# Kernel tuning notes

Hardware: AMD Instinct MI355X
Metric: run time of the kernel (lower is better)

## Reference

```python
import jax, jax.numpy as jnp
import numpy as np

# ---- module constants (from init_kwargs) ----
NOF_LINKS = 64
NOISE = 1e-3          # gen_para.input_noise_power
DT = 0.01             # gen_para.dt
T_END = 5.12          # t
TXP = 1.0             # gen_para.tx_power
LAM = 1.0
RHO = 1.0

T_ARR = jnp.arange(0.0, T_END, DT, dtype=jnp.float32)   # [T] time grid
POW2T = jnp.power(jnp.float32(2.0), T_ARR)               # 2^t
POW2T_1 = POW2T - 1.0                                    # 2^t - 1
LN2 = jnp.log(jnp.float32(2.0))


def setup_inputs() -> dict:
    key = jax.random.key(0)
    k1, k2 = jax.random.split(key)
    pathloss = jax.random.uniform(k1, (NOF_LINKS, NOF_LINKS), dtype=jnp.float32)
    powers = jax.random.uniform(k2, (16, 20, NOF_LINKS), dtype=jnp.float32)
    return {"pathloss": pathloss, "powers": powers}


def _outage(pathloss, power):
    # power: [B, N, L]; pathloss: [L, L]
    B, N, L = power.shape
    T = T_ARR.shape[0]
    # signal[b,n,i,j] = pathloss[i,j] * power[b,n,i]  (per original expand/permute)
    y_ii = jnp.diagonal(pathloss)[None, None, :] * power              # [B,N,L]
    y_tot = power * jnp.sum(pathloss, axis=1)[None, None, :]          # sum_j signal
    y_ij = y_tot - y_ii
    sinr = y_ii / (y_ij + NOISE)                                      # [B,N,L]

    # block-0 outage CDF over time grid: Q1[b,i,t] = 1 - exp(-(2^t-1) * sinr[b,0,i])
    Q1 = 1.0 - jnp.exp(-POW2T_1[None, None, :] * sinr[:, 0, :, None])  # [B,L,T]

    # per-block pdf kernels for n >= 1 (vectorized over all blocks up front)
    s = sinr[:, 1:, :, None]                                          # [B,N-1,L,1]
    q = jnp.exp(-POW2T_1 * s) * POW2T * s * LN2                       # [B,N-1,L,T]

    def step(Q, qn):
        # Q, qn: [B,L,T]; per-channel grouped cross-correlation (torch conv1d semantics)
        x = Q.reshape(1, B * L, T)
        w = qn.reshape(B * L, 1, T)
        out = jax.lax.conv_general_dilated(
            x, w, window_strides=(1,), padding=[(T - 1, T - 1)],
            feature_group_count=B * L)                                 # [1,B*L,2T-1]
        Qn = out[0, :, :T].reshape(B, L, T) * DT
        return Qn, Qn[:, :, -1]

    q_scan = jnp.moveaxis(q, 1, 0)                                    # [N-1,B,L,T]
    _, outa_rest = jax.lax.scan(step, Q1, q_scan)                     # [N-1,B,L]
    outa = jnp.concatenate([Q1[None, :, :, -1], outa_rest], axis=0)   # [N,B,L]
    return jnp.moveaxis(outa, 0, 1)                                   # [B,N,L]


def reference(pathloss, powers):
    power = powers * TXP
    N = power.shape[1]
    outa = _outage(pathloss, power)                                   # [B,N,L]
    E = power[:, 0, :] + jnp.sum(power[:, 1:, :] * outa[:, :N - 1, :], axis=1)
    D = 1.0 + jnp.sum(outa[:, :N - 1, :], axis=1)
    loss = jnp.sum(E) + LAM * jnp.sum(outa[:, N - 1, :]) + RHO * jnp.sum(D)
    return loss
```

## Files before the change

### kernel.cpp

```cpp
#include <hip/hip_runtime.h>

#define LL 64
#define NN 20
#define DTC 0.01f
#define NOISEC 1e-3f
#define LN2C 0.69314718056f

typedef __attribute__((ext_vector_type(8))) short short8x;
typedef __attribute__((ext_vector_type(4))) float f32x4;
typedef __attribute__((ext_vector_type(4))) int v4i;

__device__ __forceinline__ unsigned bf16r(float x) {
    union { float f; unsigned u; } a; a.f = x;
    return (a.u + (0x7fffu + ((a.u >> 16) & 1u))) >> 16;
}
__device__ __forceinline__ unsigned pk_bf16(float x, float y) {
    return bf16r(x) | (bf16r(y) << 16);
}

__device__ __forceinline__ short8x dpp_shr1(short8x v) {
    v4i p = __builtin_bit_cast(v4i, v);
    v4i q;
    q.x = __builtin_amdgcn_update_dpp(0, p.x, 0x111, 0xf, 0xf, true);
    q.y = __builtin_amdgcn_update_dpp(0, p.y, 0x111, 0xf, 0xf, true);
    q.z = __builtin_amdgcn_update_dpp(0, p.z, 0x111, 0xf, 0xf, true);
    q.w = __builtin_amdgcn_update_dpp(0, p.w, 0x111, 0xf, 0xf, true);
    return __builtin_bit_cast(short8x, q);
}

__global__ __launch_bounds__(64, 1) void outage_kernel(
    const float* __restrict__ pathloss,
    const float* __restrict__ powers,
    float* __restrict__ out)
{
    __shared__ __align__(16) unsigned short gt[2][8][544];
    __shared__ __align__(16) unsigned short Qb[2][1024];

    const int lane = threadIdx.x;
    const int c = blockIdx.x, b = c >> 6, l = c & 63;
    const int nh = lane & 15;
    const int qd = lane >> 4;

    const float pl = pathloss[l * LL + lane];
    float rs = pl;
    #pragma unroll
    for (int mk = 1; mk < 64; mk <<= 1) rs += __shfl_xor(rs, mk, 64);
    const float dg   = __shfl(pl, l, 64);
    const float dsum = rs - dg;

    float P2[8], P1[8];
    #pragma unroll
    for (int u = 0; u < 8; ++u) {
        P2[u] = exp2f((8 * lane + u) * DTC);
        P1[u] = P2[u] - 1.f;
    }

    *((uint4*)&Qb[0][0] + lane) = uint4{0u, 0u, 0u, 0u};
    *((uint4*)&Qb[1][0] + lane) = uint4{0u, 0u, 0u, 0u};
    {
        const int bb = lane >> 5, w = lane & 31;
        #pragma unroll
        for (int k = 0; k < 8; ++k) gt[bb][k][512 + w] = 0;
    }

    const float p0 = powers[(b * NN + 0) * LL + l];
    const float s0 = dg * p0 / (p0 * dsum + NOISEC);
    float q7;
    {
        float v[8];
        #pragma unroll
        for (int u = 0; u < 8; ++u) v[u] = 1.f - expf(-P1[u] * s0);
        q7 = v[7];
        uint4 d4 = { pk_bf16(v[0], v[1]), pk_bf16(v[2], v[3]),
                     pk_bf16(v[4], v[5]), pk_bf16(v[6], v[7]) };
        *(uint4*)&Qb[0][512 + 8 * lane] = d4;
    }

    const float p1v = powers[(b * NN + 1) * LL + l];
    float lossCh = 1.f + p0 + (p1v + 1.f) * q7;

    auto fill_g = [&](int buf, float p) {
        float s  = dg * p / (p * dsum + NOISEC);
        float cm = s * LN2C * DTC;
        unsigned F[8];
        #pragma unroll
        for (int w = 0; w < 4; ++w) {
            float a  = expf(-P1[2 * w] * s) * P2[2 * w] * cm;
            float bb = expf(-P1[2 * w + 1] * s) * P2[2 * w + 1] * cm;
            F[w] = pk_bf16(a, bb);
        }
        #pragma unroll
        for (int w = 0; w < 4; ++w) {
            unsigned t = (unsigned)__shfl_down((int)F[w], 1, 64);
            F[4 + w] = (lane == 63) ? 0u : t;
        }
        unsigned E[7];
        #pragma unroll
        for (int j = 0; j < 7; ++j) E[j] = (F[j] >> 16) | (F[j + 1] << 16);
        #pragma unroll
        for (int k = 0; k < 8; ++k) {
            uint4 d4;
            if ((k & 1) == 0) d4 = uint4{F[k / 2], F[k / 2 + 1], F[k / 2 + 2], F[k / 2 + 3]};
            else              d4 = uint4{E[k / 2], E[k / 2 + 1], E[k / 2 + 2], E[k / 2 + 3]};
            *(uint4*)&gt[buf][k][8 * lane] = d4;
        }
    };
    fill_g(1, p1v);

    const int kk    = (7 - nh) & 7;
    const int baseA = 511 - nh + 8 * qd - kk;
    const int baseB = 512 + 32 * nh + 8 * qd;
    const int dstw  = 512 + 32 * nh + 4 * qd;

    float pnext = powers[(b * NN + 2) * LL + l];

    for (int n = 1; n < NN; ++n) {
        const unsigned short* psrc = &Qb[(n + 1) & 1][0];
        const unsigned short* pg   = &gt[n & 1][kk][0];
        unsigned short* pdst       = &Qb[n & 1][0];

        float pfut = 0.f;
        if (n <= NN - 3) pfut = powers[(b * NN + n + 2) * LL + l];

        short8x Bv[16];
        Bv[0] = *(const short8x*)&psrc[baseB];
        #pragma unroll
        for (int d = 1; d < 16; ++d) Bv[d] = dpp_shr1(Bv[d - 1]);

        short8x A0v[16], A1v[16];
        #pragma unroll
        for (int d = 0; d < 16; ++d) {
            A0v[d] = *(const short8x*)&pg[baseA - 32 * d];
            A1v[d] = *(const short8x*)&pg[baseA - 32 * d - 16];
        }

        if (n < NN - 1) fill_g((n + 1) & 1, pnext);

        f32x4 acc0a = {0.f, 0.f, 0.f, 0.f}, acc0b = {0.f, 0.f, 0.f, 0.f};
        f32x4 acc1a = {0.f, 0.f, 0.f, 0.f}, acc1b = {0.f, 0.f, 0.f, 0.f};
        #pragma unroll
        for (int d = 0; d < 16; d += 2) {
            acc0a = __builtin_amdgcn_mfma_f32_16x16x32_bf16(A0v[d],     Bv[d],     acc0a, 0, 0, 0);
            acc1a = __builtin_amdgcn_mfma_f32_16x16x32_bf16(A1v[d],     Bv[d],     acc1a, 0, 0, 0);
            acc0b = __builtin_amdgcn_mfma_f32_16x16x32_bf16(A0v[d + 1], Bv[d + 1], acc0b, 0, 0, 0);
            acc1b = __builtin_amdgcn_mfma_f32_16x16x32_bf16(A1v[d + 1], Bv[d + 1], acc1b, 0, 0, 0);
        }
        f32x4 acc0 = acc0a + acc0b;
        f32x4 acc1 = acc1a + acc1b;

        *(uint2*)&pdst[dstw]      = uint2{pk_bf16(acc0.x, acc0.y), pk_bf16(acc0.z, acc0.w)};
        *(uint2*)&pdst[dstw + 16] = uint2{pk_bf16(acc1.x, acc1.y), pk_bf16(acc1.z, acc1.w)};

        float wgt = (n < NN - 1) ? (pnext + 1.f) : 1.f;
        lossCh += wgt * acc1.w;
        pnext = pfut;
    }

    if (lane == 63) atomicAdd(out, lossCh);
}

extern "C" void kernel_launch(void* const* d_in, const int* in_sizes, int n_in,
                              void* d_out, int out_size, void* d_ws, size_t ws_size,
                              hipStream_t stream) {
    const float* pathloss = (const float*)d_in[0];
    const float* powers   = (const float*)d_in[1];
    float* outp = (float*)d_out;

    (void)hipMemsetAsync(d_out, 0, sizeof(float) * out_size, stream);
    outage_kernel<<<16 * LL, 64, 0, stream>>>(pathloss, powers, outp);
}
```

Measured before the change: 89.87 us.

## Split per-channel convolution across two wavefronts with direct DPP shifts

Each block now runs two wavefronts, and each one computes half of the output MFMA tile (one of the two accumulator groups). Wavefront 0 fills the kernel buffer while both sync with __syncthreads every step. The chained DPP shift-by-1 sequence is replaced by direct row_shr by d from the base vector, which shortens the dependency chain. The aim is to halve the serial MFMA and LDS-load work per wave and raise occupancy. The cost is a block barrier per time step and the fill_g work still being serialized on one wave.

```diff
diff --git a/kernel.cpp b/kernel.cpp
--- a/kernel.cpp
+++ b/kernel.cpp
@@ -18,17 +18,18 @@
     return bf16r(x) | (bf16r(y) << 16);
 }
 
-__device__ __forceinline__ short8x dpp_shr1(short8x v) {
+template<int CTRL>
+__device__ __forceinline__ short8x dpp_shr(short8x v) {
     v4i p = __builtin_bit_cast(v4i, v);
     v4i q;
-    q.x = __builtin_amdgcn_update_dpp(0, p.x, 0x111, 0xf, 0xf, true);
-    q.y = __builtin_amdgcn_update_dpp(0, p.y, 0x111, 0xf, 0xf, true);
-    q.z = __builtin_amdgcn_update_dpp(0, p.z, 0x111, 0xf, 0xf, true);
-    q.w = __builtin_amdgcn_update_dpp(0, p.w, 0x111, 0xf, 0xf, true);
+    q.x = __builtin_amdgcn_update_dpp(0, p.x, CTRL, 0xf, 0xf, true);
+    q.y = __builtin_amdgcn_update_dpp(0, p.y, CTRL, 0xf, 0xf, true);
+    q.z = __builtin_amdgcn_update_dpp(0, p.z, CTRL, 0xf, 0xf, true);
+    q.w = __builtin_amdgcn_update_dpp(0, p.w, CTRL, 0xf, 0xf, true);
     return __builtin_bit_cast(short8x, q);
 }
 
-__global__ __launch_bounds__(64, 1) void outage_kernel(
+__global__ __launch_bounds__(128, 2) void outage_kernel(
     const float* __restrict__ pathloss,
     const float* __restrict__ powers,
     float* __restrict__ out)
@@ -36,7 +37,8 @@
     __shared__ __align__(16) unsigned short gt[2][8][544];
     __shared__ __align__(16) unsigned short Qb[2][1024];
 
-    const int lane = threadIdx.x;
+    const int lane = threadIdx.x & 63;
+    const int wid  = threadIdx.x >> 6;
     const int c = blockIdx.x, b = c >> 6, l = c & 63;
     const int nh = lane & 15;
     const int qd = lane >> 4;
@@ -55,9 +57,10 @@
         P1[u] = P2[u] - 1.f;
     }
 
-    *((uint4*)&Qb[0][0] + lane) = uint4{0u, 0u, 0u, 0u};
-    *((uint4*)&Qb[1][0] + lane) = uint4{0u, 0u, 0u, 0u};
-    {
+    if (wid == 0) {
+        *((uint4*)&Qb[0][0] + lane) = uint4{0u, 0u, 0u, 0u};
+    } else {
+        *((uint4*)&Qb[1][0] + lane) = uint4{0u, 0u, 0u, 0u};
         const int bb = lane >> 5, w = lane & 31;
         #pragma unroll
         for (int k = 0; k < 8; ++k) gt[bb][k][512 + w] = 0;
@@ -71,9 +74,11 @@
         #pragma unroll
         for (int u = 0; u < 8; ++u) v[u] = 1.f - expf(-P1[u] * s0);
         q7 = v[7];
-        uint4 d4 = { pk_bf16(v[0], v[1]), pk_bf16(v[2], v[3]),
-                     pk_bf16(v[4], v[5]), pk_bf16(v[6], v[7]) };
-        *(uint4*)&Qb[0][512 + 8 * lane] = d4;
+        if (wid == 0) {
+            uint4 d4 = { pk_bf16(v[0], v[1]), pk_bf16(v[2], v[3]),
+                         pk_bf16(v[4], v[5]), pk_bf16(v[6], v[7]) };
+            *(uint4*)&Qb[0][512 + 8 * lane] = d4;
+        }
     }
 
     const float p1v = powers[(b * NN + 1) * LL + l];
@@ -105,14 +110,17 @@
             *(uint4*)&gt[buf][k][8 * lane] = d4;
         }
     };
-    fill_g(1, p1v);
+    if (wid == 0) fill_g(1, p1v);
 
     const int kk    = (7 - nh) & 7;
     const int baseA = 511 - nh + 8 * qd - kk;
+    const int aoff  = baseA - (wid << 4);
     const int baseB = 512 + 32 * nh + 8 * qd;
-    const int dstw  = 512 + 32 * nh + 4 * qd;
+    const int dstw  = 512 + 32 * nh + 4 * qd + (wid << 4);
 
     float pnext = powers[(b * NN + 2) * LL + l];
+
+    __syncthreads();
 
     for (int n = 1; n < NN; ++n) {
         const unsigned short* psrc = &Qb[(n + 1) & 1][0];
@@ -123,40 +131,52 @@
         if (n <= NN - 3) pfut = powers[(b * NN + n + 2) * LL + l];
 
         short8x Bv[16];
-        Bv[0] = *(const short8x*)&psrc[baseB];
+        Bv[0]  = *(const short8x*)&psrc[baseB];
+        Bv[1]  = dpp_shr<0x111>(Bv[0]);
+        Bv[2]  = dpp_shr<0x112>(Bv[0]);
+        Bv[3]  = dpp_shr<0x113>(Bv[0]);
+        Bv[4]  = dpp_shr<0x114>(Bv[0]);
+        Bv[5]  = dpp_shr<0x115>(Bv[0]);
+        Bv[6]  = dpp_shr<0x116>(Bv[0]);
+        Bv[7]  = dpp_shr<0x117>(Bv[0]);
+        Bv[8]  = dpp_shr<0x118>(Bv[0]);
+        Bv[9]  = dpp_shr<0x119>(Bv[0]);
+        Bv[10] = dpp_shr<0x11A>(Bv[0]);
+        Bv[11] = dpp_shr<0x11B>(Bv[0]);
+        Bv[12] = dpp_shr<0x11C>(Bv[0]);
+        Bv[13] = dpp_shr<0x11D>(Bv[0]);
+        Bv[14] = dpp_shr<0x11E>(Bv[0]);
+        Bv[15] = dpp_shr<0x11F>(Bv[0]);
+
+        short8x Av[16];
         #pragma unroll
-        for (int d = 1; d < 16; ++d) Bv[d] = dpp_shr1(Bv[d - 1]);
+        for (int d = 0; d < 16; ++d) Av[d] = *(const short8x*)&pg[aoff - 32 * d];
 
-        short8x A0v[16], A1v[16];
+        if (wid == 0 && n < NN - 1) fill_g((n + 1) & 1, pnext);
+
+        f32x4 a0 = {0.f, 0.f, 0.f, 0.f}, a1 = {0.f, 0.f, 0.f, 0.f};
+        f32x4 a2 = {0.f, 0.f, 0.f, 0.f}, a3 = {0.f, 0.f, 0.f, 0.f};
         #pragma unroll
-        for (int d = 0; d < 16; ++d) {
-            A0v[d] = *(const short8x*)&pg[baseA - 32 * d];
-            A1v[d] = *(const short8x*)&pg[baseA - 32 * d - 16];
+        for (int d = 0; d < 16; d += 4) {
+            a0 = __builtin_amdgcn_mfma_f32_16x16x32_bf16(Av[d],     Bv[d],     a0, 0, 0, 0);
+            a1 = __builtin_amdgcn_mfma_f32_16x16x32_bf16(Av[d + 1], Bv[d + 1], a1, 0, 0, 0);
+            a2 = __builtin_amdgcn_mfma_f32_16x16x32_bf16(Av[d + 2], Bv[d + 2], a2, 0, 0, 0);
+            a3 = __builtin_amdgcn_mfma_f32_16x16x32_bf16(Av[d + 3], Bv[d + 3], a3, 0, 0, 0);
         }
+        f32x4 acc = (a0 + a1) + (a2 + a3);
 
-        if (n < NN - 1) fill_g((n + 1) & 1, pnext);
+        *(uint2*)&pdst[dstw] = uint2{pk_bf16(acc.x, acc.y), pk_bf16(acc.z, acc.w)};
 
-        f32x4 acc0a = {0.f, 0.f, 0.f, 0.f}, acc0b = {0.f, 0.f, 0.f, 0.f};
-        f32x4 acc1a = {0.f, 0.f, 0.f, 0.f}, acc1b = {0.f, 0.f, 0.f, 0.f};
-        #pragma unroll
-        for (int d = 0; d < 16; d += 2) {
-            acc0a = __builtin_amdgcn_mfma_f32_16x16x32_bf16(A0v[d],     Bv[d],     acc0a, 0, 0, 0);
-            acc1a = __builtin_amdgcn_mfma_f32_16x16x32_bf16(A1v[d],     Bv[d],     acc1a, 0, 0, 0);
-            acc0b = __builtin_amdgcn_mfma_f32_16x16x32_bf16(A0v[d + 1], Bv[d + 1], acc0b, 0, 0, 0);
-            acc1b = __builtin_amdgcn_mfma_f32_16x16x32_bf16(A1v[d + 1], Bv[d + 1], acc1b, 0, 0, 0);
+        if (wid == 1) {
+            float wgt = (n < NN - 1) ? (pnext + 1.f) : 1.f;
+            lossCh += wgt * acc.w;
         }
-        f32x4 acc0 = acc0a + acc0b;
-        f32x4 acc1 = acc1a + acc1b;
+        pnext = pfut;
 
-        *(uint2*)&pdst[dstw]      = uint2{pk_bf16(acc0.x, acc0.y), pk_bf16(acc0.z, acc0.w)};
-        *(uint2*)&pdst[dstw + 16] = uint2{pk_bf16(acc1.x, acc1.y), pk_bf16(acc1.z, acc1.w)};
-
-        float wgt = (n < NN - 1) ? (pnext + 1.f) : 1.f;
-        lossCh += wgt * acc1.w;
-        pnext = pfut;
+        __syncthreads();
     }
 
-    if (lane == 63) atomicAdd(out, lossCh);
+    if (wid == 1 && lane == 63) atomicAdd(out, lossCh);
 }
 
 extern "C" void kernel_launch(void* const* d_in, const int* in_sizes, int n_in,
@@ -167,5 +187,5 @@
     float* outp = (float*)d_out;
 
     (void)hipMemsetAsync(d_out, 0, sizeof(float) * out_size, stream);
-    outage_kernel<<<16 * LL, 64, 0, stream>>>(pathloss, powers, outp);
+    outage_kernel<<<16 * LL, 128, 0, stream>>>(pathloss, powers, outp);
 }
```

Result: no change. 90.27 us (+0.4%).
